# Optimization experiments

Measured on AMD Instinct MI355X. Metric: run time of the kernel, lower is better.

## Reference

```python
import jax, jax.numpy as jnp
import numpy as np


def _minmax_norm(m):
    # per-sample min-max normalize over all non-batch dims (channel=1, h, w)
    mn = m.min(axis=(1, 2, 3), keepdims=True)
    mx = m.max(axis=(1, 2, 3), keepdims=True)
    return (m - mn) / (mx - mn)


def setup_inputs() -> dict:
    key = jax.random.key(0)
    k1, k2, k3, k4, k5 = jax.random.split(key, 5)
    N, C, H, W = 32, 256, 56, 56
    Ce, He, We = 512, 14, 14
    return {
        "main_inputs": jax.random.normal(k1, (N, C, H, W), dtype=jnp.float32),
        "embedding_inputs": jax.random.normal(k2, (N, Ce, He, We), dtype=jnp.float32),
        "conv_w": jax.random.normal(k3, (C, Ce), dtype=jnp.float32) * (1.0 / np.sqrt(Ce)),
        "conv_b": jax.random.normal(k4, (C,), dtype=jnp.float32) * 0.01,
        "weight": jax.random.normal(k5, (), dtype=jnp.float32),
    }


def reference(main_inputs, embedding_inputs, conv_w, conv_b, weight):
    N, C, H, W = main_inputs.shape
    Ce = embedding_inputs.shape[1]
    # nn.Upsample(size=(H,W), mode='bilinear', align_corners=False) == half-pixel linear resize
    up = jax.image.resize(embedding_inputs, (N, Ce, H, W), method="linear")  # [N,Ce,H,W]
    # 1x1 conv Ce -> C
    emb = jnp.einsum("nchw,oc->nohw", up, conv_w) + conv_b[None, :, None, None]  # [N,C,H,W]
    # reshape_and_normalize_masks(squeeze=True): mean over channels, per-sample min-max
    mask = emb.mean(axis=1, keepdims=True)  # [N,1,H,W]
    mask = _minmax_norm(mask)
    # second call with squeeze=False (inference_x is None): normalize again
    mask = _minmax_norm(mask)
    s = jax.nn.sigmoid(main_inputs)
    return s * mask * weight + s
```

## Files before the change

### kernel.cpp

```cpp
#include <hip/hip_runtime.h>
#include <math.h>

#define P2_OFF     33280
#define MASK_OFF   83456

__global__ void k_mask_small(const float* __restrict__ emb,
                             const float* __restrict__ conv_w,
                             float* __restrict__ ws) {
    __shared__ float wpart[256];
    __shared__ float wl[64];
    int n  = blockIdx.x;
    int cc = blockIdx.y;
    int t  = threadIdx.x;

    int col = t & 63, rg = t >> 6;
    float a = 0.f;
    const float* wp = conv_w + (rg * 64) * 512 + cc * 64 + col;
#pragma unroll 8
    for (int k = 0; k < 64; ++k) a += wp[k * 512];
    wpart[t] = a;
    __syncthreads();
    if (t < 64) wl[t] = wpart[t] + wpart[t + 64] + wpart[t + 128] + wpart[t + 192];
    __syncthreads();

    if (t < 196) {
        const float* base = emb + (size_t)(n * 512 + cc * 64) * 196 + t;
        float acc = 0.f;
#pragma unroll 8
        for (int c = 0; c < 64; ++c) acc += base[c * 196] * wl[c];
        ws[P2_OFF + (n * 8 + cc) * 196 + t] = acc;
    }
}

__global__ void k_upsample(const float* __restrict__ wgt_p, float* __restrict__ ws) {
    __shared__ float sm[196];
    __shared__ float rmin[256], rmax[256];
    int n = blockIdx.x;
    int t = threadIdx.x;

    if (t < 196) {
        float a = 0.f;
#pragma unroll
        for (int k = 0; k < 8; ++k) a += ws[P2_OFF + (n * 8 + k) * 196 + t];
        sm[t] = a;
    }
    __syncthreads();

    float vmin = INFINITY, vmax = -INFINITY;
    for (int p = t; p < 3136; p += 256) {
        int h = p / 56, w = p % 56;
        float sy = (h + 0.5f) * 0.25f - 0.5f;
        float sx = (w + 0.5f) * 0.25f - 0.5f;
        int y0 = (int)floorf(sy); float fy = sy - (float)y0;
        int x0 = (int)floorf(sx); float fx = sx - (float)x0;
        int y1 = min(y0 + 1, 13); y0 = max(y0, 0);
        int x1 = min(x0 + 1, 13); x0 = max(x0, 0);
        float v00 = sm[y0 * 14 + x0], v01 = sm[y0 * 14 + x1];
        float v10 = sm[y1 * 14 + x0], v11 = sm[y1 * 14 + x1];
        float v = (1.f - fy) * ((1.f - fx) * v00 + fx * v01)
                +        fy  * ((1.f - fx) * v10 + fx * v11);
        vmin = fminf(vmin, v);
        vmax = fmaxf(vmax, v);
    }
    rmin[t] = vmin; rmax[t] = vmax;
    __syncthreads();
    for (int s = 128; s > 0; s >>= 1) {
        if (t < s) {
            rmin[t] = fminf(rmin[t], rmin[t + s]);
            rmax[t] = fmaxf(rmax[t], rmax[t + s]);
        }
        __syncthreads();
    }
    float mn = rmin[0], mx = rmax[0];
    float a = wgt_p[0] / (mx - mn);
    float b = 1.f - mn * a;

    for (int p = t; p < 3136; p += 256) {
        int h = p / 56, w = p % 56;
        float sy = (h + 0.5f) * 0.25f - 0.5f;
        float sx = (w + 0.5f) * 0.25f - 0.5f;
        int y0 = (int)floorf(sy); float fy = sy - (float)y0;
        int x0 = (int)floorf(sx); float fx = sx - (float)x0;
        int y1 = min(y0 + 1, 13); y0 = max(y0, 0);
        int x1 = min(x0 + 1, 13); x0 = max(x0, 0);
        float v00 = sm[y0 * 14 + x0], v01 = sm[y0 * 14 + x1];
        float v10 = sm[y1 * 14 + x0], v11 = sm[y1 * 14 + x1];
        float v = (1.f - fy) * ((1.f - fx) * v00 + fx * v01)
                +        fy  * ((1.f - fx) * v10 + fx * v11);
        ws[MASK_OFF + n * 3136 + p] = v * a + b;
    }
}

__global__ void __launch_bounds__(256) k_final(const float4* __restrict__ x4,
                                               const float* __restrict__ ws,
                                               float4* __restrict__ out4) {
    const int t = threadIdx.x;
    const int s = blockIdx.x;
    const int n = blockIdx.y;
    const float4* m4 = (const float4*)(ws + MASK_OFF) + n * 784;

    const long base = (long)n * 200704 + (long)s * 2048;
    const float4* xp = x4   + base;
    float4*       op = out4 + base;

    int q = (s * 480 + t) % 784;

#pragma unroll
    for (int i = 0; i < 8; ++i) {
        float4 x = xp[i * 256 + t];
        float4 m = m4[q];
        float4 o;
        o.x = m.x * __builtin_amdgcn_rcpf(1.f + __expf(-x.x));
        o.y = m.y * __builtin_amdgcn_rcpf(1.f + __expf(-x.y));
        o.z = m.z * __builtin_amdgcn_rcpf(1.f + __expf(-x.z));
        o.w = m.w * __builtin_amdgcn_rcpf(1.f + __expf(-x.w));
        op[i * 256 + t] = o;
        q += 256;
        if (q >= 784) q -= 784;
    }
}

extern "C" void kernel_launch(void* const* d_in, const int* in_sizes, int n_in,
                              void* d_out, int out_size, void* d_ws, size_t ws_size,
                              hipStream_t stream) {
    const float* main_in = (const float*)d_in[0];
    const float* emb_in  = (const float*)d_in[1];
    const float* conv_w  = (const float*)d_in[2];
    const float* weight  = (const float*)d_in[4];

    float* ws   = (float*)d_ws;
    float4* out = (float4*)d_out;

    k_mask_small<<<dim3(32, 8),  256, 0, stream>>>(emb_in, conv_w, ws);
    k_upsample  <<<32,           256, 0, stream>>>(weight, ws);
    k_final     <<<dim3(98, 32), 256, 0, stream>>>((const float4*)main_in, ws, out);
}
```

Before: 49.10 us.

## Fuse upsample and min-max normalization into final elementwise kernel

```diff
diff --git a/kernel.cpp b/kernel.cpp
--- a/kernel.cpp
+++ b/kernel.cpp
@@ -1,8 +1,7 @@
 #include <hip/hip_runtime.h>
 #include <math.h>
 
-#define P2_OFF     33280
-#define MASK_OFF   83456
+#define P2_OFF 0
 
 __global__ void k_mask_small(const float* __restrict__ emb,
                              const float* __restrict__ conv_w,
@@ -32,11 +31,25 @@
     }
 }
 
-__global__ void k_upsample(const float* __restrict__ wgt_p, float* __restrict__ ws) {
+__global__ void __launch_bounds__(256) k_final(const float4* __restrict__ x4,
+                                               const float* __restrict__ ws,
+                                               const float* __restrict__ wgt_p,
+                                               float4* __restrict__ out4) {
     __shared__ float sm[196];
-    __shared__ float rmin[256], rmax[256];
-    int n = blockIdx.x;
-    int t = threadIdx.x;
+    __shared__ float wred[8];
+    const int t = threadIdx.x;
+    const int s = blockIdx.x;
+    const int n = blockIdx.y;
+
+    const long base = (long)n * 200704 + (long)s * 2048;
+    const float4* xp = x4   + base;
+    float4*       op = out4 + base;
+
+    float wgt = wgt_p[0];
+
+    float4 x[8];
+#pragma unroll
+    for (int i = 0; i < 8; ++i) x[i] = xp[i * 256 + t];
 
     if (t < 196) {
         float a = 0.f;
@@ -62,61 +75,51 @@
         vmin = fminf(vmin, v);
         vmax = fmaxf(vmax, v);
     }
-    rmin[t] = vmin; rmax[t] = vmax;
+#pragma unroll
+    for (int off = 32; off > 0; off >>= 1) {
+        vmin = fminf(vmin, __shfl_xor(vmin, off, 64));
+        vmax = fmaxf(vmax, __shfl_xor(vmax, off, 64));
+    }
+    if ((t & 63) == 0) { wred[t >> 6] = vmin; wred[4 + (t >> 6)] = vmax; }
     __syncthreads();
-    for (int s = 128; s > 0; s >>= 1) {
-        if (t < s) {
-            rmin[t] = fminf(rmin[t], rmin[t + s]);
-            rmax[t] = fmaxf(rmax[t], rmax[t + s]);
-        }
-        __syncthreads();
-    }
-    float mn = rmin[0], mx = rmax[0];
-    float a = wgt_p[0] / (mx - mn);
+    float mn = fminf(fminf(wred[0], wred[1]), fminf(wred[2], wred[3]));
+    float mx = fmaxf(fmaxf(wred[4], wred[5]), fmaxf(wred[6], wred[7]));
+    float a = wgt / (mx - mn);
     float b = 1.f - mn * a;
 
-    for (int p = t; p < 3136; p += 256) {
-        int h = p / 56, w = p % 56;
-        float sy = (h + 0.5f) * 0.25f - 0.5f;
-        float sx = (w + 0.5f) * 0.25f - 0.5f;
-        int y0 = (int)floorf(sy); float fy = sy - (float)y0;
-        int x0 = (int)floorf(sx); float fx = sx - (float)x0;
-        int y1 = min(y0 + 1, 13); y0 = max(y0, 0);
-        int x1 = min(x0 + 1, 13); x0 = max(x0, 0);
-        float v00 = sm[y0 * 14 + x0], v01 = sm[y0 * 14 + x1];
-        float v10 = sm[y1 * 14 + x0], v11 = sm[y1 * 14 + x1];
-        float v = (1.f - fy) * ((1.f - fx) * v00 + fx * v01)
-                +        fy  * ((1.f - fx) * v10 + fx * v11);
-        ws[MASK_OFF + n * 3136 + p] = v * a + b;
-    }
-}
-
-__global__ void __launch_bounds__(256) k_final(const float4* __restrict__ x4,
-                                               const float* __restrict__ ws,
-                                               float4* __restrict__ out4) {
-    const int t = threadIdx.x;
-    const int s = blockIdx.x;
-    const int n = blockIdx.y;
-    const float4* m4 = (const float4*)(ws + MASK_OFF) + n * 784;
-
-    const long base = (long)n * 200704 + (long)s * 2048;
-    const float4* xp = x4   + base;
-    float4*       op = out4 + base;
-
-    int q = (s * 480 + t) % 784;
+    const int q0 = (s * 480 + t) % 784;
 
 #pragma unroll
     for (int i = 0; i < 8; ++i) {
-        float4 x = xp[i * 256 + t];
-        float4 m = m4[q];
+        const int ci = (i * 256) % 784;
+        int q = q0 + ci;
+        if (q >= 784) q -= 784;
+        int r  = (q * 4682) >> 16;
+        int wq = q - r * 14;
+        float sy = r * 0.25f - 0.375f;
+        int y0 = (int)floorf(sy);
+        float fy = sy - (float)y0;
+        int y1 = min(y0 + 1, 13); y0 = max(y0, 0);
+        int xm  = max(wq - 1, 0);
+        int xp1 = min(wq + 1, 13);
+        float t0 = sm[y0 * 14 + xm], t1 = sm[y0 * 14 + wq], t2 = sm[y0 * 14 + xp1];
+        float b0 = sm[y1 * 14 + xm], b1 = sm[y1 * 14 + wq], b2 = sm[y1 * 14 + xp1];
+        float m0t = t0 + 0.625f * (t1 - t0), m0b = b0 + 0.625f * (b1 - b0);
+        float m1t = t0 + 0.875f * (t1 - t0), m1b = b0 + 0.875f * (b1 - b0);
+        float m2t = t1 + 0.125f * (t2 - t1), m2b = b1 + 0.125f * (b2 - b1);
+        float m3t = t1 + 0.375f * (t2 - t1), m3b = b1 + 0.375f * (b2 - b1);
+        float m0 = m0t + fy * (m0b - m0t);
+        float m1 = m1t + fy * (m1b - m1t);
+        float m2 = m2t + fy * (m2b - m2t);
+        float m3 = m3t + fy * (m3b - m3t);
+
+        float4 xi = x[i];
         float4 o;
-        o.x = m.x * __builtin_amdgcn_rcpf(1.f + __expf(-x.x));
-        o.y = m.y * __builtin_amdgcn_rcpf(1.f + __expf(-x.y));
-        o.z = m.z * __builtin_amdgcn_rcpf(1.f + __expf(-x.z));
-        o.w = m.w * __builtin_amdgcn_rcpf(1.f + __expf(-x.w));
+        o.x = (m0 * a + b) * __builtin_amdgcn_rcpf(1.f + __expf(-xi.x));
+        o.y = (m1 * a + b) * __builtin_amdgcn_rcpf(1.f + __expf(-xi.y));
+        o.z = (m2 * a + b) * __builtin_amdgcn_rcpf(1.f + __expf(-xi.z));
+        o.w = (m3 * a + b) * __builtin_amdgcn_rcpf(1.f + __expf(-xi.w));
         op[i * 256 + t] = o;
-        q += 256;
-        if (q >= 784) q -= 784;
     }
 }
 
@@ -132,6 +135,5 @@
     float4* out = (float4*)d_out;
 
     k_mask_small<<<dim3(32, 8),  256, 0, stream>>>(emb_in, conv_w, ws);
-    k_upsample  <<<32,           256, 0, stream>>>(weight, ws);
-    k_final     <<<dim3(98, 32), 256, 0, stream>>>((const float4*)main_in, ws, out);
+    k_final     <<<dim3(98, 32), 256, 0, stream>>>((const float4*)main_in, ws, weight, out);
 }
```

Result: faster. 46.36 us (median of 2 runs) (-5.6%).
